# Kernel optimization log

Hardware: AMD Instinct MI355X
Metric: run time of the kernel (lower is better)

The kernel has to match this reference:

```python
import jax, jax.numpy as jnp
import numpy as np

N, E = 50000, 800000
DIN, DOUT = 256, 128
DH = 2 * DOUT  # hidden width of conv1


def setup_inputs() -> dict:
    key = jax.random.key(0)
    ks = jax.random.split(key, 9)
    x = jax.random.normal(ks[0], (N, DIN), dtype=jnp.float32)
    edge_index = jax.random.randint(ks[1], (2, E), 0, N, dtype=jnp.int64)
    edge_weight = jax.random.uniform(ks[2], (E,), dtype=jnp.float32)
    s1 = 1.0 / np.sqrt(DIN)
    s2 = 1.0 / np.sqrt(DH)
    W1 = jax.random.uniform(ks[3], (DIN, DH), minval=-s1, maxval=s1, dtype=jnp.float32)
    b1 = jnp.zeros((DH,), jnp.float32)
    Wmu = jax.random.uniform(ks[4], (DH, DOUT), minval=-s2, maxval=s2, dtype=jnp.float32)
    bmu = jnp.zeros((DOUT,), jnp.float32)
    Wls = jax.random.uniform(ks[5], (DH, DOUT), minval=-s2, maxval=s2, dtype=jnp.float32)
    bls = jnp.zeros((DOUT,), jnp.float32)
    return {"x": x, "edge_index": edge_index, "edge_weight": edge_weight,
            "W1": W1, "b1": b1, "Wmu": Wmu, "bmu": bmu, "Wls": Wls, "bls": bls}


def _gcn_layer(x, row, col, norm, W, b, n):
    # GCNConv: linear transform, then normalized scatter-add aggregation, then bias
    h = x @ W                                   # [N, Dout]
    msg = h[row] * norm[:, None]                # gather source feats, scale per-edge
    agg = jax.ops.segment_sum(msg, col, num_segments=n)  # scatter-add to targets
    return agg + b


def reference(x, edge_index, edge_weight, W1, b1, Wmu, bmu, Wls, bls):
    n = x.shape[0]
    row, col = edge_index[0], edge_index[1]
    # add self loops with weight 1 (PyG gcn_norm default, fill_value=1)
    loop = jnp.arange(n)
    row_f = jnp.concatenate([row, loop])
    col_f = jnp.concatenate([col, loop])
    ew = jnp.concatenate([edge_weight, jnp.ones((n,), x.dtype)])
    # symmetric normalization: deg computed over destination index
    deg = jax.ops.segment_sum(ew, col_f, num_segments=n)
    dinv = jnp.where(deg > 0, jax.lax.rsqrt(deg), 0.0)
    norm = dinv[row_f] * ew * dinv[col_f]       # cached=True -> same norm each layer
    h = jax.nn.relu(_gcn_layer(x, row_f, col_f, norm, W1, b1, n))
    mu = _gcn_layer(h, row_f, col_f, norm, Wmu, bmu, n)
    logstd = _gcn_layer(h, row_f, col_f, norm, Wls, bls, n)
    return mu, logstd
```

## Files before the change

### kernel.cpp

```cpp
#include <hip/hip_runtime.h>

#define THREADS 256

typedef __attribute__((ext_vector_type(8))) short bf16x8;
typedef __attribute__((ext_vector_type(4))) float f32x4;
typedef __attribute__((ext_vector_type(4))) int i32x4;

#define CNT_SHIFT 20
#define DEG_SCALE 8192.0f
#define DEG_MASK  ((1u << CNT_SHIFT) - 1)

__device__ inline float bf2f(unsigned short u) {
    union { unsigned int i; float f; } v; v.i = ((unsigned int)u) << 16; return v.f;
}
__device__ inline unsigned short f2bf(float f) {
    union { float f; unsigned int i; } v; v.f = f;
    unsigned int i = v.i;
    i += 0x7fff + ((i >> 16) & 1);
    return (unsigned short)(i >> 16);
}

__global__ void k_scan_part(const unsigned int* __restrict__ packed,
                            int* __restrict__ counts, float* __restrict__ dinv,
                            int* __restrict__ offsets, int* __restrict__ blocksum, int n) {
    __shared__ int s[THREADS];
    int i = blockIdx.x * THREADS + threadIdx.x;
    unsigned int p = (i < n) ? packed[i] : 0u;
    int v = (int)(p >> CNT_SHIFT);
    if (i < n) {
        counts[i] = v;
        float d = 1.0f + (float)(p & DEG_MASK) * (1.0f / DEG_SCALE);
        dinv[i] = rsqrtf(d);
    }
    s[threadIdx.x] = v;
    __syncthreads();
    for (int d = 1; d < THREADS; d <<= 1) {
        int t = (threadIdx.x >= d) ? s[threadIdx.x - d] : 0;
        __syncthreads();
        s[threadIdx.x] += t;
        __syncthreads();
    }
    if (i < n) offsets[i] = s[threadIdx.x] - v;
    if (threadIdx.x == THREADS - 1) blocksum[blockIdx.x] = s[THREADS - 1];
}

__global__ void k_scan_block(int* __restrict__ blocksum, int nb) {
    __shared__ int s[THREADS];
    int v = (threadIdx.x < nb) ? blocksum[threadIdx.x] : 0;
    s[threadIdx.x] = v;
    __syncthreads();
    for (int d = 1; d < THREADS; d <<= 1) {
        int t = (threadIdx.x >= d) ? s[threadIdx.x - d] : 0;
        __syncthreads();
        s[threadIdx.x] += t;
        __syncthreads();
    }
    if (threadIdx.x < nb) blocksum[threadIdx.x] = s[threadIdx.x] - v;
}

__global__ void k_fill(const int* __restrict__ ei, const float* __restrict__ ew,
                       const float* __restrict__ dinv, const int* __restrict__ offsets,
                       const int* __restrict__ bsum,
                       const int* __restrict__ rank, int2* __restrict__ epack, int E) {
    int e = blockIdx.x * THREADS + threadIdx.x;
    if (e >= E) return;
    int r = __builtin_nontemporal_load(ei + e);
    int c = __builtin_nontemporal_load(ei + E + e);
    float w = __builtin_nontemporal_load(ew + e);
    int rk = __builtin_nontemporal_load(rank + e);
    int pos = offsets[c] + bsum[c >> 8] + rk;
    long long m = (long long)r |
        ((long long)__float_as_int(dinv[r] * w * dinv[c]) << 32);
    __builtin_nontemporal_store(m, (long long*)&epack[pos]);
}

__global__ void k_cvt_w(const float* __restrict__ W1, const float* __restrict__ Wmu,
                        const float* __restrict__ Wls, const float* __restrict__ bmu,
                        const float* __restrict__ bls,
                        ushort* __restrict__ W1t, ushort* __restrict__ Wct,
                        float* __restrict__ bcat, unsigned int* __restrict__ packed,
                        int n) {
    int nb = blockIdx.x, k = threadIdx.x;
    int gi = nb * THREADS + k;
    if (gi < n) packed[gi] = 0u;
    if (nb < 256) {
        W1t[k * 256 + nb] = f2bf(W1[nb * 256 + k]);
    } else if (nb < 512) {
        int r = nb - 256;
        float v = (k < 128) ? Wmu[r * 128 + k] : Wls[r * 128 + (k - 128)];
        Wct[k * 256 + r] = f2bf(v);
    } else {
        bcat[k] = (k < 128) ? bmu[k] : bls[k - 128];
    }
}

template<int MODE>
__global__ void k_agg(const ushort4* __restrict__ fb,
                      const int* __restrict__ eoff, const int* __restrict__ ecnt,
                      const int* __restrict__ bsum,
                      const int2* __restrict__ epack, const float* __restrict__ dinv,
                      const float* __restrict__ bias, void* __restrict__ out, int n) {
    int wave = threadIdx.x >> 6, lane = threadIdx.x & 63;
    int node = blockIdx.x * 4 + wave;
    if (node >= n) return;
    float ds = dinv[node]; ds *= ds;
    ushort4 v = fb[(size_t)node * 64 + lane];
    float ax = ds * bf2f(v.x), ay = ds * bf2f(v.y),
          az = ds * bf2f(v.z), aw = ds * bf2f(v.w);
    int e = eoff[node] + bsum[node >> 8], cnt = ecnt[node];
    while (cnt > 0) {
        int take = cnt < 64 ? cnt : 64;
        int2 meta = make_int2(0, 0);
        if (lane < take) {
            long long m = __builtin_nontemporal_load((const long long*)&epack[e + lane]);
            meta.x = (int)m; meta.y = (int)(m >> 32);
        }
        for (int j = 0; j < take; j += 8) {
            int s0 = __builtin_amdgcn_readlane(meta.x, j + 0);
            int s1 = __builtin_amdgcn_readlane(meta.x, j + 1);
            int s2 = __builtin_amdgcn_readlane(meta.x, j + 2);
            int s3 = __builtin_amdgcn_readlane(meta.x, j + 3);
            int s4 = __builtin_amdgcn_readlane(meta.x, j + 4);
            int s5 = __builtin_amdgcn_readlane(meta.x, j + 5);
            int s6 = __builtin_amdgcn_readlane(meta.x, j + 6);
            int s7 = __builtin_amdgcn_readlane(meta.x, j + 7);
            float w0 = __int_as_float(__builtin_amdgcn_readlane(meta.y, j + 0));
            float w1 = __int_as_float(__builtin_amdgcn_readlane(meta.y, j + 1));
            float w2 = __int_as_float(__builtin_amdgcn_readlane(meta.y, j + 2));
            float w3 = __int_as_float(__builtin_amdgcn_readlane(meta.y, j + 3));
            float w4 = __int_as_float(__builtin_amdgcn_readlane(meta.y, j + 4));
            float w5 = __int_as_float(__builtin_amdgcn_readlane(meta.y, j + 5));
            float w6 = __int_as_float(__builtin_amdgcn_readlane(meta.y, j + 6));
            float w7 = __int_as_float(__builtin_amdgcn_readlane(meta.y, j + 7));
            ushort4 u0 = fb[(size_t)s0 * 64 + lane];
            ushort4 u1 = fb[(size_t)s1 * 64 + lane];
            ushort4 u2 = fb[(size_t)s2 * 64 + lane];
            ushort4 u3 = fb[(size_t)s3 * 64 + lane];
            ushort4 u4 = fb[(size_t)s4 * 64 + lane];
            ushort4 u5 = fb[(size_t)s5 * 64 + lane];
            ushort4 u6 = fb[(size_t)s6 * 64 + lane];
            ushort4 u7 = fb[(size_t)s7 * 64 + lane];
            ax += w0 * bf2f(u0.x) + w1 * bf2f(u1.x) + w2 * bf2f(u2.x) + w3 * bf2f(u3.x);
            ay += w0 * bf2f(u0.y) + w1 * bf2f(u1.y) + w2 * bf2f(u2.y) + w3 * bf2f(u3.y);
            az += w0 * bf2f(u0.z) + w1 * bf2f(u1.z) + w2 * bf2f(u2.z) + w3 * bf2f(u3.z);
            aw += w0 * bf2f(u0.w) + w1 * bf2f(u1.w) + w2 * bf2f(u2.w) + w3 * bf2f(u3.w);
            ax += w4 * bf2f(u4.x) + w5 * bf2f(u5.x) + w6 * bf2f(u6.x) + w7 * bf2f(u7.x);
            ay += w4 * bf2f(u4.y) + w5 * bf2f(u5.y) + w6 * bf2f(u6.y) + w7 * bf2f(u7.y);
            az += w4 * bf2f(u4.z) + w5 * bf2f(u5.z) + w6 * bf2f(u6.z) + w7 * bf2f(u7.z);
            aw += w4 * bf2f(u4.w) + w5 * bf2f(u5.w) + w6 * bf2f(u6.w) + w7 * bf2f(u7.w);
        }
        e += take; cnt -= take;
    }
    float4 b = ((const float4*)bias)[lane];
    ax += b.x; ay += b.y; az += b.z; aw += b.w;
    if (MODE == 0) {
        unsigned long long o =
            (unsigned long long)f2bf(fmaxf(ax, 0.f)) |
            ((unsigned long long)f2bf(fmaxf(ay, 0.f)) << 16) |
            ((unsigned long long)f2bf(fmaxf(az, 0.f)) << 32) |
            ((unsigned long long)f2bf(fmaxf(aw, 0.f)) << 48);
        __builtin_nontemporal_store(o, (unsigned long long*)out + (size_t)node * 64 + lane);
    } else {
        f32x4 o; o[0] = ax; o[1] = ay; o[2] = az; o[3] = aw;
        f32x4* mu = (f32x4*)out;
        f32x4* ls = mu + (size_t)n * 32;
        if (lane < 32) __builtin_nontemporal_store(o, &mu[(size_t)node * 32 + lane]);
        else           __builtin_nontemporal_store(o, &ls[(size_t)node * 32 + (lane - 32)]);
    }
}

#define LDT 40
template<int AF32>
__device__ __forceinline__ void gemm_body(const void* __restrict__ Ain,
        const ushort* __restrict__ Bt, ushort* __restrict__ C, int M, int bid) {
    __shared__ ushort As[128 * LDT];
    __shared__ ushort Bs[256 * LDT];
    const float*  Af = (const float*)Ain;
    const ushort* Ab = (const ushort*)Ain;
    int tid = threadIdx.x;
    int lane = tid & 63, wave = tid >> 6;
    int row0 = bid * 128;
    int mw = (wave >> 2) * 64, nw = (wave & 3) * 64;
    int lr = lane & 15, lq = lane >> 4;
    f32x4 acc[4][4] = {};
    for (int k0 = 0; k0 < 256; k0 += 32) {
        {
            int r = tid >> 2, q = tid & 3;
            int gr = row0 + r;
            i32x4 av = {0, 0, 0, 0};
            if (gr < M) {
                if (AF32) {
                    const float* p = Af + (size_t)gr * 256 + k0 + q * 8;
                    i32x4 lo = __builtin_nontemporal_load((const i32x4*)p);
                    i32x4 hi = __builtin_nontemporal_load((const i32x4*)(p + 4));
                    ushort* u = (ushort*)&av;
                    u[0] = f2bf(__int_as_float(lo[0])); u[1] = f2bf(__int_as_float(lo[1]));
                    u[2] = f2bf(__int_as_float(lo[2])); u[3] = f2bf(__int_as_float(lo[3]));
                    u[4] = f2bf(__int_as_float(hi[0])); u[5] = f2bf(__int_as_float(hi[1]));
                    u[6] = f2bf(__int_as_float(hi[2])); u[7] = f2bf(__int_as_float(hi[3]));
                } else {
                    av = __builtin_nontemporal_load(
                        (const i32x4*)(Ab + (size_t)gr * 256 + k0 + q * 8));
                }
            }
            *(i32x4*)(&As[r * LDT + q * 8]) = av;
        }
        #pragma unroll
        for (int i = 0; i < 2; i++) {
            int c = tid + i * 512;
            int r = c >> 2, q = c & 3;
            i32x4 bv = *(const i32x4*)(Bt + (size_t)r * 256 + k0 + q * 8);
            *(i32x4*)(&Bs[r * LDT + q * 8]) = bv;
        }
        __syncthreads();
        bf16x8 af[4], bfr[4];
        #pragma unroll
        for (int mi = 0; mi < 4; mi++)
            af[mi] = *(const bf16x8*)(&As[(mw + mi * 16 + lr) * LDT + lq * 8]);
        #pragma unroll
        for (int ni = 0; ni < 4; ni++)
            bfr[ni] = *(const bf16x8*)(&Bs[(nw + ni * 16 + lr) * LDT + lq * 8]);
        #pragma unroll
        for (int mi = 0; mi < 4; mi++)
            #pragma unroll
            for (int ni = 0; ni < 4; ni++)
                acc[mi][ni] = __builtin_amdgcn_mfma_f32_16x16x32_bf16(
                    af[mi], bfr[ni], acc[mi][ni], 0, 0, 0);
        __syncthreads();
    }
    #pragma unroll
    for (int mi = 0; mi < 4; mi++)
        #pragma unroll
        for (int ni = 0; ni < 4; ni++)
            #pragma unroll
            for (int r = 0; r < 4; r++) {
                int grow = row0 + mw + mi * 16 + lq * 4 + r;
                int gcol = nw + ni * 16 + lr;
                if (grow < M) C[(size_t)grow * 256 + gcol] = f2bf(acc[mi][ni][r]);
            }
}

template<int AF32>
__global__ __launch_bounds__(512) void k_gemm(const void* __restrict__ Ain,
        const ushort* __restrict__ Bt, ushort* __restrict__ C, int M) {
    gemm_body<AF32>(Ain, Bt, C, M, blockIdx.x);
}

__global__ __launch_bounds__(512) void k_gemm1_count(
        const float* __restrict__ x, const ushort* __restrict__ W1t,
        ushort* __restrict__ C, int M, int nGemm,
        const int* __restrict__ dst, const float* __restrict__ ew,
        unsigned int* __restrict__ packed, int* __restrict__ rank, int E) {
    int bid = blockIdx.x;
    if (bid < nGemm) {
        gemm_body<1>(x, W1t, C, M, bid);
        return;
    }
    int e = (bid - nGemm) * 512 + threadIdx.x;
    if (e >= E) return;
    int c = __builtin_nontemporal_load(dst + e);
    float w = __builtin_nontemporal_load(ew + e);
    unsigned int v = (1u << CNT_SHIFT) | (unsigned int)(w * DEG_SCALE + 0.5f);
    unsigned int old = atomicAdd(&packed[c], v);
    __builtin_nontemporal_store((int)(old >> CNT_SHIFT), rank + e);
}

extern "C" void kernel_launch(void* const* d_in, const int* in_sizes, int n_in,
                              void* d_out, int out_size, void* d_ws, size_t ws_size,
                              hipStream_t stream) {
    const float* x   = (const float*)d_in[0];
    const int*   ei  = (const int*)d_in[1];
    const float* ew  = (const float*)d_in[2];
    const float* W1  = (const float*)d_in[3];
    const float* b1  = (const float*)d_in[4];
    const float* Wmu = (const float*)d_in[5];
    const float* bmu = (const float*)d_in[6];
    const float* Wls = (const float*)d_in[7];
    const float* bls = (const float*)d_in[8];

    const int DIN = 256;
    const int N = in_sizes[0] / DIN;
    const int E = in_sizes[2];

    unsigned int* packed = (unsigned int*)d_ws;
    int*   counts   = (int*)(packed + N);
    int*   offsets  = counts + N;
    float* dinv     = (float*)(offsets + N);
    int*   blocksum = (int*)(dinv + N);
    int*   rank     = blocksum + 256;
    int2*  epack    = (int2*)(rank + E);
    ushort* xw      = (ushort*)(epack + E);
    ushort* hb      = xw + (size_t)N * 256;
    ushort* hw      = hb + (size_t)N * 256;
    ushort* W1t     = hw + (size_t)N * 256;
    ushort* Wct     = W1t + 256 * 256;
    float*  bcat    = (float*)(Wct + 256 * 256);

    int gN = (N + THREADS - 1) / THREADS;
    int gE = (E + THREADS - 1) / THREADS;

    k_cvt_w<<<513, THREADS, 0, stream>>>(W1, Wmu, Wls, bmu, bls, W1t, Wct, bcat,
                                         packed, N);

    int nGemm = (N + 127) / 128;
    int nCnt  = (E + 511) / 512;

    k_gemm1_count<<<nGemm + nCnt, 512, 0, stream>>>(x, W1t, xw, N, nGemm,
                                                    ei + E, ew, packed, rank, E);

    k_scan_part<<<gN, THREADS, 0, stream>>>(packed, counts, dinv, offsets, blocksum, N);
    k_scan_block<<<1, THREADS, 0, stream>>>(blocksum, gN);

    k_fill<<<gE, THREADS, 0, stream>>>(ei, ew, dinv, offsets, blocksum, rank, epack, E);

    int gAgg = (N + 3) / 4;

    k_agg<0><<<gAgg, THREADS, 0, stream>>>((const ushort4*)xw, offsets, counts,
                                           blocksum, epack, dinv, b1, hb, N);

    k_gemm<0><<<nGemm, 512, 0, stream>>>(hb, Wct, hw, N);
    k_agg<1><<<gAgg, THREADS, 0, stream>>>((const ushort4*)hw, offsets, counts,
                                           blocksum, epack, dinv, bcat, d_out, N);
}
```

Before: 327.0 us.

## Overlap edge CSR fill with first GEMM instead of degree counting

Moves the edge degree-count atomics into the weight-conversion kernel and fuses the CSR fill pass with the first dense GEMM launch, so the GEMM now overlaps with the fill rather than with counting. This removes one kernel launch and lets the scan run before the GEMM. Zeroing of the packed counters moves to a hipMemsetAsync, and the epack store changes from nontemporal to a normal store. The scan kernels now sit between count and GEMM, so they become a serial gap that the GEMM can no longer hide.

```diff
diff --git a/kernel.cpp b/kernel.cpp
--- a/kernel.cpp
+++ b/kernel.cpp
@@ -18,6 +18,34 @@
     unsigned int i = v.i;
     i += 0x7fff + ((i >> 16) & 1);
     return (unsigned short)(i >> 16);
+}
+
+__global__ void k_cvt_count(const float* __restrict__ W1, const float* __restrict__ Wmu,
+                            const float* __restrict__ Wls, const float* __restrict__ bmu,
+                            const float* __restrict__ bls,
+                            ushort* __restrict__ W1t, ushort* __restrict__ Wct,
+                            float* __restrict__ bcat,
+                            const int* __restrict__ dst, const float* __restrict__ ew,
+                            unsigned int* __restrict__ packed,
+                            int* __restrict__ rank, int E) {
+    int nb = blockIdx.x, k = threadIdx.x;
+    if (nb < 256) {
+        W1t[k * 256 + nb] = f2bf(W1[nb * 256 + k]);
+    } else if (nb < 512) {
+        int r = nb - 256;
+        float v = (k < 128) ? Wmu[r * 128 + k] : Wls[r * 128 + (k - 128)];
+        Wct[k * 256 + r] = f2bf(v);
+    } else if (nb == 512) {
+        bcat[k] = (k < 128) ? bmu[k] : bls[k - 128];
+    } else {
+        int e = (nb - 513) * THREADS + k;
+        if (e >= E) return;
+        int c = __builtin_nontemporal_load(dst + e);
+        float w = __builtin_nontemporal_load(ew + e);
+        unsigned int v = (1u << CNT_SHIFT) | (unsigned int)(w * DEG_SCALE + 0.5f);
+        unsigned int old = atomicAdd(&packed[c], v);
+        __builtin_nontemporal_store((int)(old >> CNT_SHIFT), rank + e);
+    }
 }
 
 __global__ void k_scan_part(const unsigned int* __restrict__ packed,
@@ -56,42 +84,6 @@
         __syncthreads();
     }
     if (threadIdx.x < nb) blocksum[threadIdx.x] = s[threadIdx.x] - v;
-}
-
-__global__ void k_fill(const int* __restrict__ ei, const float* __restrict__ ew,
-                       const float* __restrict__ dinv, const int* __restrict__ offsets,
-                       const int* __restrict__ bsum,
-                       const int* __restrict__ rank, int2* __restrict__ epack, int E) {
-    int e = blockIdx.x * THREADS + threadIdx.x;
-    if (e >= E) return;
-    int r = __builtin_nontemporal_load(ei + e);
-    int c = __builtin_nontemporal_load(ei + E + e);
-    float w = __builtin_nontemporal_load(ew + e);
-    int rk = __builtin_nontemporal_load(rank + e);
-    int pos = offsets[c] + bsum[c >> 8] + rk;
-    long long m = (long long)r |
-        ((long long)__float_as_int(dinv[r] * w * dinv[c]) << 32);
-    __builtin_nontemporal_store(m, (long long*)&epack[pos]);
-}
-
-__global__ void k_cvt_w(const float* __restrict__ W1, const float* __restrict__ Wmu,
-                        const float* __restrict__ Wls, const float* __restrict__ bmu,
-                        const float* __restrict__ bls,
-                        ushort* __restrict__ W1t, ushort* __restrict__ Wct,
-                        float* __restrict__ bcat, unsigned int* __restrict__ packed,
-                        int n) {
-    int nb = blockIdx.x, k = threadIdx.x;
-    int gi = nb * THREADS + k;
-    if (gi < n) packed[gi] = 0u;
-    if (nb < 256) {
-        W1t[k * 256 + nb] = f2bf(W1[nb * 256 + k]);
-    } else if (nb < 512) {
-        int r = nb - 256;
-        float v = (k < 128) ? Wmu[r * 128 + k] : Wls[r * 128 + (k - 128)];
-        Wct[k * 256 + r] = f2bf(v);
-    } else {
-        bcat[k] = (k < 128) ? bmu[k] : bls[k - 128];
-    }
 }
 
 template<int MODE>
@@ -246,11 +238,13 @@
     gemm_body<AF32>(Ain, Bt, C, M, blockIdx.x);
 }
 
-__global__ __launch_bounds__(512) void k_gemm1_count(
+__global__ __launch_bounds__(512) void k_gemm1_fill(
         const float* __restrict__ x, const ushort* __restrict__ W1t,
         ushort* __restrict__ C, int M, int nGemm,
-        const int* __restrict__ dst, const float* __restrict__ ew,
-        unsigned int* __restrict__ packed, int* __restrict__ rank, int E) {
+        const int* __restrict__ ei, const float* __restrict__ ew,
+        const float* __restrict__ dinv, const int* __restrict__ offsets,
+        const int* __restrict__ bsum, const int* __restrict__ rank,
+        int2* __restrict__ epack, int E) {
     int bid = blockIdx.x;
     if (bid < nGemm) {
         gemm_body<1>(x, W1t, C, M, bid);
@@ -258,11 +252,14 @@
     }
     int e = (bid - nGemm) * 512 + threadIdx.x;
     if (e >= E) return;
-    int c = __builtin_nontemporal_load(dst + e);
+    int r = __builtin_nontemporal_load(ei + e);
+    int c = __builtin_nontemporal_load(ei + E + e);
     float w = __builtin_nontemporal_load(ew + e);
-    unsigned int v = (1u << CNT_SHIFT) | (unsigned int)(w * DEG_SCALE + 0.5f);
-    unsigned int old = atomicAdd(&packed[c], v);
-    __builtin_nontemporal_store((int)(old >> CNT_SHIFT), rank + e);
+    int rk = __builtin_nontemporal_load(rank + e);
+    int pos = offsets[c] + bsum[c >> 8] + rk;
+    long long m = (long long)r |
+        ((long long)__float_as_int(dinv[r] * w * dinv[c]) << 32);
+    *(long long*)&epack[pos] = m;
 }
 
 extern "C" void kernel_launch(void* const* d_in, const int* in_sizes, int n_in,
@@ -297,21 +294,23 @@
     float*  bcat    = (float*)(Wct + 256 * 256);
 
     int gN = (N + THREADS - 1) / THREADS;
-    int gE = (E + THREADS - 1) / THREADS;
-
-    k_cvt_w<<<513, THREADS, 0, stream>>>(W1, Wmu, Wls, bmu, bls, W1t, Wct, bcat,
-                                         packed, N);
-
-    int nGemm = (N + 127) / 128;
-    int nCnt  = (E + 511) / 512;
-
-    k_gemm1_count<<<nGemm + nCnt, 512, 0, stream>>>(x, W1t, xw, N, nGemm,
+
+    hipMemsetAsync(packed, 0, (size_t)N * sizeof(unsigned int), stream);
+
+    int nCnt = (E + THREADS - 1) / THREADS;
+    k_cvt_count<<<513 + nCnt, THREADS, 0, stream>>>(W1, Wmu, Wls, bmu, bls,
+                                                    W1t, Wct, bcat,
                                                     ei + E, ew, packed, rank, E);
 
     k_scan_part<<<gN, THREADS, 0, stream>>>(packed, counts, dinv, offsets, blocksum, N);
     k_scan_block<<<1, THREADS, 0, stream>>>(blocksum, gN);
 
-    k_fill<<<gE, THREADS, 0, stream>>>(ei, ew, dinv, offsets, blocksum, rank, epack, E);
+    int nGemm = (N + 127) / 128;
+    int nFill = (E + 511) / 512;
+
+    k_gemm1_fill<<<nGemm + nFill, 512, 0, stream>>>(x, W1t, xw, N, nGemm,
+                                                    ei, ew, dinv, offsets,
+                                                    blocksum, rank, epack, E);
 
     int gAgg = (N + 3) / 4;
 
```

After: 325.1 us (median of 2 runs). Within noise of the previous version (-0.6%).
